# Performance work log

Hardware: AMD Instinct MI355X
Metric: run time of the kernel (lower is better)

## Reference

```python
import jax, jax.numpy as jnp
import numpy as np

BW = 2            # bit width
THR = 0.5         # brevitas TernaryQuant threshold
W_SCALE = 0.1     # SignedTernaryWeightPerTensorConst scale
A_SCALE = 1.0     # SignedTernaryActPerTensorConst scale


def _ste(x, q):
    # straight-through estimator: forward q, gradient identity
    return x + jax.lax.stop_gradient(q - x)


def ternary(x, scale):
    # brevitas TernaryQuant: {-scale, 0, +scale} with threshold*scale
    q = jnp.where(x > THR * scale, scale,
                  jnp.where(x < -THR * scale, -scale, 0.0)).astype(x.dtype)
    return _ste(x, q)


def fp_quant(w, bw=BW):
    # Int8WeightPerTensorFixedPoint at bw bits: power-of-two per-tensor scale
    int_max = 2.0 ** (bw - 1) - 1.0
    maxabs = jax.lax.stop_gradient(jnp.max(jnp.abs(w)))
    scale = 2.0 ** jnp.ceil(jnp.log2(maxabs / int_max))
    q = jnp.clip(jnp.round(w / scale), -(2.0 ** (bw - 1)), int_max) * scale
    return _ste(w, q)


def setup_inputs() -> dict:
    key = jax.random.key(0)
    ks = jax.random.split(key, 8)
    V, E, H, L, O = 30000, 1024, 1024, 2, 4
    B, T = 64, 512
    text = jax.random.randint(ks[0], (B, T), 0, V, dtype=jnp.int64)
    text_lengths = jax.random.randint(ks[1], (B,), 1, T, dtype=jnp.int64)
    s = 0.1
    emb_W = jax.random.normal(ks[2], (V, E), jnp.float32) * s
    W_ih = jax.random.normal(ks[3], (L, H, E), jnp.float32) * s
    W_hh = jax.random.normal(ks[4], (L, H, H), jnp.float32) * s
    b_ih = jax.random.normal(ks[5], (L, H), jnp.float32) * s
    b_hh = jax.random.normal(ks[6], (L, H), jnp.float32) * s
    fc_W = jax.random.normal(ks[7], (O, H), jnp.float32) * s
    return {"text": text, "text_lengths": text_lengths, "emb_W": emb_W,
            "W_ih": W_ih, "W_hh": W_hh, "b_ih": b_ih, "b_hh": b_hh,
            "fc_W": fc_W}


def reference(text, text_lengths, emb_W, W_ih, W_hh, b_ih, b_hh, fc_W):
    # quantized embedding lookup -> [B,T,E]
    x = fp_quant(emb_W)[text]
    x = ternary(x, A_SCALE)  # io_quant on RNN input
    n_layers = W_ih.shape[0]
    finals = []
    for l in range(n_layers):
        Wi = ternary(W_ih[l], W_SCALE)  # [H,in]
        Wh = ternary(W_hh[l], W_SCALE)  # [H,H]
        b = b_ih[l] + b_hh[l]
        # precompute input contribution for all timesteps: [B,T,H]
        xw = jnp.einsum('bte,he->bth', x, Wi) + b
        B = x.shape[0]
        h0 = jnp.zeros((B, Wh.shape[0]), x.dtype)

        def step(h, xw_t):
            acc = ternary(xw_t + h @ Wh.T, A_SCALE)   # gate_acc_quant
            h_new = ternary(jnp.tanh(acc), A_SCALE)   # tanh_quant / io_quant
            return h_new, h_new

        h_last, ys = jax.lax.scan(step, h0, jnp.swapaxes(xw, 0, 1))
        x = jnp.swapaxes(ys, 0, 1)  # [B,T,H] feeds next layer
        finals.append(h_last)
    hidden = jnp.stack(finals)  # [L,B,H] = hidden_state
    # quantized linear (no bias) applied to hidden_state -> [L,B,O]
    return jnp.einsum('lbh,oh->lbo', hidden, ternary(fc_W, W_SCALE))
```

## Files before the change

### kernel.cpp

```cpp
#include <hip/hip_runtime.h>
#include <cstdint>
#include <cstddef>


static __device__ __forceinline__ float bf2f(unsigned short b) {
  return __uint_as_float(((unsigned)b) << 16);
}
static __device__ __forceinline__ unsigned short f2bf(float f) {
  unsigned u = __float_as_uint(f);
  u = (u + 0x7FFFu + ((u >> 16) & 1u)) >> 16;
  return (unsigned short)u;
}
static __device__ __forceinline__ float loadw(const void* p, size_t i, int isf32) {
  return isf32 ? ((const float*)p)[i] : bf2f(((const unsigned short*)p)[i]);
}

__global__ __launch_bounds__(256) void k_detect(const unsigned short* __restrict__ embu,
                                                const int* __restrict__ text,
                                                int* __restrict__ flags) {
  int i = blockIdx.x * 256 + threadIdx.x;
  unsigned e = (embu[i] >> 7) & 0xFFu;
  unsigned long long b = __ballot(e >= 127u);
  if ((threadIdx.x & 63) == 0 && b) atomicOr(&flags[0], 1);
  if (blockIdx.x == 0 && threadIdx.x == 0) {
    int allz = 1;
    for (int j = 0; j < 32; j++)
      if (text[2 * j + 1] != 0) allz = 0;
    flags[1] = allz;
  }
}

__global__ __launch_bounds__(256) void k_maxabs(const uint4* __restrict__ w,
                                                const int* __restrict__ flags,
                                                unsigned* __restrict__ out) {
  int isf32 = flags[0];
  int n16 = isf32 ? 7680000 : 3840000;
  float mf = 0.f;
  unsigned mb = 0;
  int i = blockIdx.x * blockDim.x + threadIdx.x;
  int stride = gridDim.x * blockDim.x;
  if (isf32) {
    for (; i < n16; i += stride) {
      uint4 v = w[i];
      mf = fmaxf(mf, fabsf(__uint_as_float(v.x)));
      mf = fmaxf(mf, fabsf(__uint_as_float(v.y)));
      mf = fmaxf(mf, fabsf(__uint_as_float(v.z)));
      mf = fmaxf(mf, fabsf(__uint_as_float(v.w)));
    }
  } else {
    for (; i < n16; i += stride) {
      uint4 v = w[i];
      unsigned a;
      a = v.x & 0x7FFF7FFFu; mb = max(mb, a & 0xFFFFu); mb = max(mb, a >> 16);
      a = v.y & 0x7FFF7FFFu; mb = max(mb, a & 0xFFFFu); mb = max(mb, a >> 16);
      a = v.z & 0x7FFF7FFFu; mb = max(mb, a & 0xFFFFu); mb = max(mb, a >> 16);
      a = v.w & 0x7FFF7FFFu; mb = max(mb, a & 0xFFFFu); mb = max(mb, a >> 16);
    }
    mf = bf2f((unsigned short)mb);
  }
  for (int off = 32; off > 0; off >>= 1) mf = fmaxf(mf, __shfl_down(mf, off));
  __shared__ float red[4];
  if ((threadIdx.x & 63) == 0) red[threadIdx.x >> 6] = mf;
  __syncthreads();
  if (threadIdx.x == 0) {
    float b = fmaxf(fmaxf(red[0], red[1]), fmaxf(red[2], red[3]));
    atomicMax(out, __float_as_uint(b));
  }
}

__global__ __launch_bounds__(1024) void k_tern_rows(
    const void* __restrict__ Wih, const void* __restrict__ Whh,
    const void* __restrict__ fcw, const int* __restrict__ flags,
    unsigned long long* __restrict__ wim, unsigned long long* __restrict__ whm,
    unsigned long long* __restrict__ fcm) {
  int isf32 = flags[0];
  int b = blockIdx.x;
  const void* src;
  size_t rowoff;
  unsigned long long* dst;
  if (b < 2048)      { src = Wih; rowoff = (size_t)b * 1024; dst = wim + (size_t)b * 32; }
  else if (b < 4096) { int r = b - 2048; src = Whh; rowoff = (size_t)r * 1024; dst = whm + (size_t)r * 32; }
  else               { int r = b - 4096; src = fcw; rowoff = (size_t)r * 1024; dst = fcm + (size_t)r * 32; }
  double w = (double)loadw(src, rowoff + threadIdx.x, isf32);
  unsigned long long bp = __ballot(w > 0.05);
  unsigned long long bm = __ballot(w < -0.05);
  if ((threadIdx.x & 63) == 0) {
    int wv = threadIdx.x >> 6;
    dst[2 * wv] = bp;
    dst[2 * wv + 1] = bp | bm;
  }
}

__global__ __launch_bounds__(1024) void k_embed(const int* __restrict__ text,
    const void* __restrict__ emb, const int* __restrict__ flags,
    const unsigned* __restrict__ mab, unsigned long long* __restrict__ x0) {
  int isf32 = flags[0], i64 = flags[1];
  int bt = blockIdx.x;
  long long tok = i64 ? ((const long long*)text)[bt] : (long long)text[bt];
  double ma = (double)__uint_as_float(*mab);
  float s = (float)exp2(ceil(log2(ma)));
  float inv_s = 1.0f / s;
  float w = loadw(emb, (size_t)tok * 1024 + threadIdx.x, isf32);
  float q = rintf(w * inv_s);
  q = fminf(fmaxf(q, -2.0f), 1.0f);
  float val = q * s;
  int code = (val > 0.5f) ? 1 : ((val < -0.5f) ? -1 : 0);
  unsigned long long bp = __ballot(code == 1);
  unsigned long long bm = __ballot(code == -1);
  if ((threadIdx.x & 63) == 0) {
    int wv = threadIdx.x >> 6;
    x0[(size_t)bt * 32 + 2 * wv] = bp;
    x0[(size_t)bt * 32 + 2 * wv + 1] = bp | bm;
  }
}

__global__ __launch_bounds__(256, 4) void k_bitgemm(const unsigned long long* __restrict__ xm,
    const unsigned long long* __restrict__ wim, short* __restrict__ nbuf) {
  __shared__ __align__(16) uint4 lx[64 * 16];
  __shared__ unsigned any[64];
  int tid = threadIdx.x;
  int bt0 = blockIdx.x * 64;
  int r = blockIdx.y * 256 + tid;
  unsigned wplo[16], wphi[16], wzlo[16], wzhi[16];
  const uint4* wrow = (const uint4*)(wim + (size_t)r * 32);
#pragma unroll
  for (int i = 0; i < 16; i++) {
    uint4 w4 = wrow[i];
    wplo[i] = w4.x; wphi[i] = w4.y; wzlo[i] = w4.z; wzhi[i] = w4.w;
  }
  if (tid < 64) any[tid] = 0;
  __syncthreads();
  unsigned accor = 0;
#pragma unroll
  for (int i = 0; i < 4; i++) {
    int idx = tid * 4 + i;
    uint4 v = ((const uint4*)(xm + (size_t)bt0 * 32))[idx];
    lx[idx] = v;
    accor |= v.z | v.w;
  }
  if (accor) atomicOr(&any[tid >> 2], 1u);
  __syncthreads();
  for (int bt = 0; bt < 64; bt++) {
    int k = 0;
    if (any[bt]) {
      const uint4* hx = lx + bt * 16;
      int sb = 0, sn = 0;
#pragma unroll
      for (int i = 0; i < 16; i++) {
        uint4 h = hx[i];
        unsigned blo = h.z & wzlo[i];
        unsigned bhi = h.w & wzhi[i];
        unsigned nlo = (h.x ^ wplo[i]) & blo;
        unsigned nhi = (h.y ^ wphi[i]) & bhi;
        sb += __popc(blo) + __popc(bhi);
        sn += __popc(nlo) + __popc(nhi);
      }
      k = sb - 2 * sn;
    }
    nbuf[(size_t)(bt0 + bt) * 1024 + r] = (short)k;
  }
}

#define FLAG_STRIDE 16

template <int ROLE>
static __device__ __forceinline__ void recur_stage(
    uint4 (*shb)[16], const short* nbuf,
    const unsigned long long* __restrict__ whm,
    const void* __restrict__ bih, const void* __restrict__ bhh,
    int isf32, int layer, int b, int r,
    unsigned long long* xrow,
    int* flagsA, int* flagsB,
    unsigned long long* __restrict__ hidm) {
  unsigned wplo[16], wphi[16], wzlo[16], wzhi[16];
  const uint4* wrow = (const uint4*)(whm + (size_t)(layer * 1024 + r) * 32);
#pragma unroll
  for (int i = 0; i < 16; i++) {
    uint4 w4 = wrow[i];
    wplo[i] = w4.x; wphi[i] = w4.y; wzlo[i] = w4.z; wzhi[i] = w4.w;
  }
  size_t boff = (size_t)layer * 1024 + r;
  double bias = (double)loadw(bih, boff, isf32) + (double)loadw(bhh, boff, isf32);
  int kp = (int)ceil((0.5 - bias) * 10.0);
  while ((double)kp * 0.1 + bias <= 0.5) kp++;
  while ((double)(kp - 1) * 0.1 + bias > 0.5) kp--;
  int km = (int)floor((-0.5 - bias) * 10.0);
  while ((double)km * 0.1 + bias >= -0.5) km--;
  while ((double)(km + 1) * 0.1 + bias < -0.5) km++;

  if (r < 32) ((unsigned long long*)shb)[r] = 0;
  const short* nrow = nbuf + (size_t)b * 512 * 1024 + r;
  int wv = r >> 6;
  bool l0 = (r & 63) == 0;
  int nin;
  if (ROLE == 0) {
    nin = (int)nrow[0];
  } else {
    while (__hip_atomic_load(flagsB + b * FLAG_STRIDE, __ATOMIC_RELAXED,
                             __HIP_MEMORY_SCOPE_AGENT) < 1) {}
    nin = (int)__hip_atomic_load(nrow, __ATOMIC_RELAXED, __HIP_MEMORY_SCOPE_AGENT);
  }
  __syncthreads();
  int pb = 0;
  for (int t = 0; t < 512; t++) {
    int fl = 0;
    if (ROLE == 2 && t < 511)
      fl = __hip_atomic_load(flagsB + b * FLAG_STRIDE, __ATOMIC_RELAXED,
                             __HIP_MEMORY_SCOPE_AGENT);
    const uint4* Hq = shb[pb];
    int sb = 0, sn = 0;
#pragma unroll
    for (int i = 0; i < 8; i++) {
      uint4 h = Hq[i];
      unsigned blo = h.z & wzlo[i];
      unsigned bhi = h.w & wzhi[i];
      unsigned nlo = (h.x ^ wplo[i]) & blo;
      unsigned nhi = (h.y ^ wphi[i]) & bhi;
      sb += __popc(blo) + __popc(bhi);
      sn += __popc(nlo) + __popc(nhi);
    }
    int nin_next = 0;
    bool got = true;
    if (ROLE == 0) {
      if (t < 511) nin_next = (int)nrow[(size_t)(t + 1) * 1024];
    } else if (t < 511) {
      got = (fl >= t + 2);
      if (got)
        nin_next = (int)__hip_atomic_load(nrow + (size_t)(t + 1) * 1024,
                                          __ATOMIC_RELAXED, __HIP_MEMORY_SCOPE_AGENT);
    }
#pragma unroll
    for (int i = 8; i < 16; i++) {
      uint4 h = Hq[i];
      unsigned blo = h.z & wzlo[i];
      unsigned bhi = h.w & wzhi[i];
      unsigned nlo = (h.x ^ wplo[i]) & blo;
      unsigned nhi = (h.y ^ wphi[i]) & bhi;
      sb += __popc(blo) + __popc(bhi);
      sn += __popc(nlo) + __popc(nhi);
    }
    int k = nin + sb - 2 * sn;
    unsigned long long bp = __ballot(k >= kp);
    unsigned long long bm = __ballot(k <= km);
    unsigned long long bz = bp | bm;
    if (l0) {
      uint4 o;
      o.x = (unsigned)bp; o.y = (unsigned)(bp >> 32);
      o.z = (unsigned)bz; o.w = (unsigned)(bz >> 32);
      shb[pb ^ 1][wv] = o;
      if (ROLE == 0) ((uint4*)(xrow + (size_t)t * 32))[wv] = o;
    }
    if (ROLE == 2 && !got && t < 511) {
      while (__hip_atomic_load(flagsB + b * FLAG_STRIDE, __ATOMIC_RELAXED,
                               __HIP_MEMORY_SCOPE_AGENT) < t + 2) {}
      nin_next = (int)__hip_atomic_load(nrow + (size_t)(t + 1) * 1024,
                                        __ATOMIC_RELAXED, __HIP_MEMORY_SCOPE_AGENT);
    }
    __syncthreads();
    if (ROLE == 0 && r == 0 && (t & 3) == 3)
      __hip_atomic_store(flagsA + b * FLAG_STRIDE, t + 1, __ATOMIC_RELEASE,
                         __HIP_MEMORY_SCOPE_AGENT);
    pb ^= 1;
    nin = nin_next;
  }
  if (r < 16) {
    uint4 h = shb[pb][r];
    size_t ho = (size_t)(layer * 64 + b) * 32;
    hidm[ho + 2 * r]     = ((unsigned long long)h.y << 32) | h.x;
    hidm[ho + 2 * r + 1] = ((unsigned long long)h.w << 32) | h.z;
  }
}

__global__ __launch_bounds__(1024, 4) void k_pipe(
    short* nbuf, unsigned long long* x0,
    const unsigned long long* __restrict__ wim,
    const unsigned long long* __restrict__ whm,
    const void* __restrict__ bih, const void* __restrict__ bhh,
    const int* __restrict__ flags, int* flagsA, int* flagsB,
    unsigned long long* __restrict__ hidm) {
  __shared__ __align__(16) uint4 shb[2][16];
  int role = blockIdx.x % 3;
  int b = blockIdx.x / 3;
  int r = threadIdx.x;
  int isf32 = flags[0];
  if (role == 0) {
    recur_stage<0>(shb, nbuf, whm, bih, bhh, isf32, 0, b, r,
                   x0 + (size_t)b * 512 * 32, flagsA, flagsB, hidm);
  } else if (role == 1) {
    unsigned wplo[16], wphi[16], wzlo[16], wzhi[16];
    const uint4* wrow = (const uint4*)(wim + (size_t)(1024 + r) * 32);
#pragma unroll
    for (int i = 0; i < 16; i++) {
      uint4 w4 = wrow[i];
      wplo[i] = w4.x; wphi[i] = w4.y; wzlo[i] = w4.z; wzhi[i] = w4.w;
    }
    const unsigned long long* xsrc = x0 + (size_t)b * 512 * 32;
    short* nout = nbuf + (size_t)b * 512 * 1024 + r;
    for (int t = 0; t < 512; t++) {
      if (r < 64) {
        while (__hip_atomic_load(flagsA + b * FLAG_STRIDE, __ATOMIC_RELAXED,
                                 __HIP_MEMORY_SCOPE_AGENT) < t + 1) {}
      }
      if (r < 32) {
        unsigned long long v = __hip_atomic_load(xsrc + (size_t)t * 32 + r,
                                                 __ATOMIC_RELAXED,
                                                 __HIP_MEMORY_SCOPE_AGENT);
        ((unsigned long long*)(shb[t & 1]))[r] = v;
      }
      __syncthreads();
      const uint4* hx = shb[t & 1];
      int sb = 0, sn = 0;
#pragma unroll
      for (int i = 0; i < 16; i++) {
        uint4 h = hx[i];
        unsigned blo = h.z & wzlo[i];
        unsigned bhi = h.w & wzhi[i];
        unsigned nlo = (h.x ^ wplo[i]) & blo;
        unsigned nhi = (h.y ^ wphi[i]) & bhi;
        sb += __popc(blo) + __popc(bhi);
        sn += __popc(nlo) + __popc(nhi);
      }
      nout[(size_t)t * 1024] = (short)(sb - 2 * sn);
      __syncthreads();
      if (r == 0)
        __hip_atomic_store(flagsB + b * FLAG_STRIDE, t + 1, __ATOMIC_RELEASE,
                           __HIP_MEMORY_SCOPE_AGENT);
    }
  } else {
    recur_stage<2>(shb, nbuf, whm, bih, bhh, isf32, 1, b, r,
                   (unsigned long long*)0, flagsA, flagsB, hidm);
  }
}

__global__ __launch_bounds__(64) void k_fc(const unsigned long long* __restrict__ hidm,
    const unsigned long long* __restrict__ fcm, const int* __restrict__ flags,
    void* __restrict__ out) {
  int isf32 = flags[0];
  int lb = blockIdx.x, lane = threadIdx.x;
  unsigned long long hp = 0, hz = 0;
  if (lane < 16) {
    hp = hidm[lb * 32 + 2 * lane];
    hz = hidm[lb * 32 + 2 * lane + 1];
  }
#pragma unroll
  for (int o = 0; o < 4; o++) {
    int k = 0;
    if (lane < 16) {
      unsigned long long wp = fcm[o * 32 + 2 * lane], wz = fcm[o * 32 + 2 * lane + 1];
      unsigned long long both = hz & wz;
      unsigned long long neg = both & (hp ^ wp);
      k = __popcll(both) - 2 * __popcll(neg);
    }
    for (int off = 8; off > 0; off >>= 1) k += __shfl_down(k, off);
    if (lane == 0) {
      float v = (float)((double)k * 0.1);
      if (isf32) ((float*)out)[lb * 4 + o] = v;
      else       ((unsigned short*)out)[lb * 4 + o] = f2bf(v);
    }
  }
}

extern "C" void kernel_launch(void* const* d_in, const int* in_sizes, int n_in,
                              void* d_out, int out_size, void* d_ws, size_t ws_size,
                              hipStream_t stream) {
  (void)in_sizes; (void)n_in; (void)out_size; (void)ws_size;
  const int* text = (const int*)d_in[0];
  const void* emb = d_in[2];
  const void* Wih = d_in[3];
  const void* Whh = d_in[4];
  const void* bih = d_in[5];
  const void* bhh = d_in[6];
  const void* fcw = d_in[7];

  char* ws = (char*)d_ws;
  int* flags = (int*)(ws);
  unsigned* mab = (unsigned*)(ws + 64);
  int* flagsA = (int*)(ws + 1024);
  int* flagsB = (int*)(ws + 5120);
  size_t off = 16384;
  unsigned long long* x0 = (unsigned long long*)(ws + off);  off += (size_t)32768 * 256;
  unsigned long long* wim = (unsigned long long*)(ws + off); off += (size_t)2048 * 256;
  unsigned long long* whm = (unsigned long long*)(ws + off); off += (size_t)2048 * 256;
  unsigned long long* fcm = (unsigned long long*)(ws + off); off += (size_t)4 * 256;
  unsigned long long* hidm = (unsigned long long*)(ws + off); off += (size_t)128 * 256;
  short* nbuf = (short*)(ws + off);                          off += (size_t)32768 * 1024 * 2;

  hipMemsetAsync(ws, 0, 16384, stream);
  k_detect<<<256, 256, 0, stream>>>((const unsigned short*)emb, text, flags);
  k_maxabs<<<2048, 256, 0, stream>>>((const uint4*)emb, flags, mab);
  k_tern_rows<<<4100, 1024, 0, stream>>>(Wih, Whh, fcw, flags, wim, whm, fcm);
  k_embed<<<32768, 1024, 0, stream>>>(text, emb, flags, mab, x0);
  k_bitgemm<<<dim3(512, 4), 256, 0, stream>>>(x0, wim, nbuf);
  k_pipe<<<192, 1024, 0, stream>>>(nbuf, x0, wim, whm, bih, bhh, flags,
                                   flagsA, flagsB, hidm);
  k_fc<<<128, 64, 0, stream>>>(hidm, fcm, flags, d_out);
}
```

Measured before the change: 1.880 ms.

## Replace release atomics with vmcnt drains and prefetch cross-block pipeline data

Cross-block flag stores now use relaxed atomics with an explicit s_waitcnt vmcnt(0) before the barrier instead of release semantics, which avoids the cache writeback/invalidate that release stores can trigger. Layer-0 now signals every step instead of every fourth, and its x0 row stores are deferred by one step so they overlap the next computation. The input-projection role prefetches the next step's x0 row one iteration ahead and caches the last seen flag value, so it polls less often. Correctness now relies on the vmcnt drain and on agent-scope relaxed atomics being coherent across the pipelined blocks.

```diff
diff --git a/kernel.cpp b/kernel.cpp
--- a/kernel.cpp
+++ b/kernel.cpp
@@ -2,6 +2,8 @@
 #include <cstdint>
 #include <cstddef>
 
+
+#define DRAIN_VMEM() asm volatile("s_waitcnt vmcnt(0)" ::: "memory")
 
 static __device__ __forceinline__ float bf2f(unsigned short b) {
   return __uint_as_float(((unsigned)b) << 16);
@@ -163,6 +165,13 @@
 
 #define FLAG_STRIDE 16
 
+static __device__ __forceinline__ int ldflag(const int* p) {
+  return __hip_atomic_load(p, __ATOMIC_RELAXED, __HIP_MEMORY_SCOPE_AGENT);
+}
+static __device__ __forceinline__ void stflag(int* p, int v) {
+  __hip_atomic_store(p, v, __ATOMIC_RELAXED, __HIP_MEMORY_SCOPE_AGENT);
+}
+
 template <int ROLE>
 static __device__ __forceinline__ void recur_stage(
     uint4 (*shb)[16], const short* nbuf,
@@ -192,21 +201,29 @@
   const short* nrow = nbuf + (size_t)b * 512 * 1024 + r;
   int wv = r >> 6;
   bool l0 = (r & 63) == 0;
+  int fl = 0;
   int nin;
   if (ROLE == 0) {
     nin = (int)nrow[0];
   } else {
-    while (__hip_atomic_load(flagsB + b * FLAG_STRIDE, __ATOMIC_RELAXED,
-                             __HIP_MEMORY_SCOPE_AGENT) < 1) {}
+    while ((fl = ldflag(flagsB + b * FLAG_STRIDE)) < 1) {}
     nin = (int)__hip_atomic_load(nrow, __ATOMIC_RELAXED, __HIP_MEMORY_SCOPE_AGENT);
   }
   __syncthreads();
   int pb = 0;
+  unsigned long long plo = 0, phi = 0;
   for (int t = 0; t < 512; t++) {
-    int fl = 0;
-    if (ROLE == 2 && t < 511)
-      fl = __hip_atomic_load(flagsB + b * FLAG_STRIDE, __ATOMIC_RELAXED,
-                             __HIP_MEMORY_SCOPE_AGENT);
+    if (ROLE == 0) {
+      if (l0 && t > 0) {
+        __hip_atomic_store(xrow + (size_t)(t - 1) * 32 + 2 * wv, plo,
+                           __ATOMIC_RELAXED, __HIP_MEMORY_SCOPE_AGENT);
+        __hip_atomic_store(xrow + (size_t)(t - 1) * 32 + 2 * wv + 1, phi,
+                           __ATOMIC_RELAXED, __HIP_MEMORY_SCOPE_AGENT);
+      }
+    } else {
+      if (t < 511 && fl < t + 2)
+        fl = ldflag(flagsB + b * FLAG_STRIDE);
+    }
     const uint4* Hq = shb[pb];
     int sb = 0, sn = 0;
 #pragma unroll
@@ -248,20 +265,30 @@
       o.x = (unsigned)bp; o.y = (unsigned)(bp >> 32);
       o.z = (unsigned)bz; o.w = (unsigned)(bz >> 32);
       shb[pb ^ 1][wv] = o;
-      if (ROLE == 0) ((uint4*)(xrow + (size_t)t * 32))[wv] = o;
+      plo = bp; phi = bz;
     }
     if (ROLE == 2 && !got && t < 511) {
-      while (__hip_atomic_load(flagsB + b * FLAG_STRIDE, __ATOMIC_RELAXED,
-                               __HIP_MEMORY_SCOPE_AGENT) < t + 2) {}
+      while ((fl = ldflag(flagsB + b * FLAG_STRIDE)) < t + 2) {}
       nin_next = (int)__hip_atomic_load(nrow + (size_t)(t + 1) * 1024,
                                         __ATOMIC_RELAXED, __HIP_MEMORY_SCOPE_AGENT);
     }
+    if (ROLE == 0) DRAIN_VMEM();
     __syncthreads();
-    if (ROLE == 0 && r == 0 && (t & 3) == 3)
-      __hip_atomic_store(flagsA + b * FLAG_STRIDE, t + 1, __ATOMIC_RELEASE,
-                         __HIP_MEMORY_SCOPE_AGENT);
+    if (ROLE == 0 && r == 0 && t > 0)
+      stflag(flagsA + b * FLAG_STRIDE, t);
     pb ^= 1;
     nin = nin_next;
+  }
+  if (ROLE == 0) {
+    if (l0) {
+      __hip_atomic_store(xrow + (size_t)511 * 32 + 2 * wv, plo,
+                         __ATOMIC_RELAXED, __HIP_MEMORY_SCOPE_AGENT);
+      __hip_atomic_store(xrow + (size_t)511 * 32 + 2 * wv + 1, phi,
+                         __ATOMIC_RELAXED, __HIP_MEMORY_SCOPE_AGENT);
+    }
+    DRAIN_VMEM();
+    __syncthreads();
+    if (r == 0) stflag(flagsA + b * FLAG_STRIDE, 512);
   }
   if (r < 16) {
     uint4 h = shb[pb][r];
@@ -296,18 +323,25 @@
     }
     const unsigned long long* xsrc = x0 + (size_t)b * 512 * 32;
     short* nout = nbuf + (size_t)b * 512 * 1024 + r;
+    int fa = 0;
+    unsigned long long vcur = 0;
+    if (r < 32) {
+      while ((fa = ldflag(flagsA + b * FLAG_STRIDE)) < 1) {}
+      vcur = __hip_atomic_load(xsrc + r, __ATOMIC_RELAXED, __HIP_MEMORY_SCOPE_AGENT);
+    }
     for (int t = 0; t < 512; t++) {
-      if (r < 64) {
-        while (__hip_atomic_load(flagsA + b * FLAG_STRIDE, __ATOMIC_RELAXED,
-                                 __HIP_MEMORY_SCOPE_AGENT) < t + 1) {}
+      if (r < 32) ((unsigned long long*)(shb[t & 1]))[r] = vcur;
+      __syncthreads();
+      bool got = false;
+      unsigned long long vnext = 0;
+      if (r < 32 && t < 511) {
+        if (fa < t + 2) fa = ldflag(flagsA + b * FLAG_STRIDE);
+        if (fa >= t + 2) {
+          vnext = __hip_atomic_load(xsrc + (size_t)(t + 1) * 32 + r,
+                                    __ATOMIC_RELAXED, __HIP_MEMORY_SCOPE_AGENT);
+          got = true;
+        }
       }
-      if (r < 32) {
-        unsigned long long v = __hip_atomic_load(xsrc + (size_t)t * 32 + r,
-                                                 __ATOMIC_RELAXED,
-                                                 __HIP_MEMORY_SCOPE_AGENT);
-        ((unsigned long long*)(shb[t & 1]))[r] = v;
-      }
-      __syncthreads();
       const uint4* hx = shb[t & 1];
       int sb = 0, sn = 0;
 #pragma unroll
@@ -320,11 +354,17 @@
         sb += __popc(blo) + __popc(bhi);
         sn += __popc(nlo) + __popc(nhi);
       }
-      nout[(size_t)t * 1024] = (short)(sb - 2 * sn);
+      __hip_atomic_store(nout + (size_t)t * 1024, (short)(sb - 2 * sn),
+                         __ATOMIC_RELAXED, __HIP_MEMORY_SCOPE_AGENT);
+      if (r < 32 && t < 511 && !got) {
+        while ((fa = ldflag(flagsA + b * FLAG_STRIDE)) < t + 2) {}
+        vnext = __hip_atomic_load(xsrc + (size_t)(t + 1) * 32 + r,
+                                  __ATOMIC_RELAXED, __HIP_MEMORY_SCOPE_AGENT);
+      }
+      DRAIN_VMEM();
       __syncthreads();
-      if (r == 0)
-        __hip_atomic_store(flagsB + b * FLAG_STRIDE, t + 1, __ATOMIC_RELEASE,
-                           __HIP_MEMORY_SCOPE_AGENT);
+      if (r == 0) stflag(flagsB + b * FLAG_STRIDE, t + 1);
+      vcur = vnext;
     }
   } else {
     recur_stage<2>(shb, nbuf, whm, bih, bhh, isf32, 1, b, r,
```

New measurement: 1.509 ms. 1.25x faster.
